# Kernel optimization log

Measured on AMD Instinct MI355X. Metric: run time of the kernel, lower is better.

## Reference

```python
import jax, jax.numpy as jnp
import numpy as np

N_HEADS, D_MODEL, D_HEAD = 16, 1024, 64
INIT_STD = 0.02


def setup_inputs() -> dict:
    key = jax.random.key(0)
    ks = jax.random.split(key, 5)
    x = jax.random.normal(ks[0], (4, 2048, D_MODEL), dtype=jnp.float32)
    W_Q = jax.random.normal(ks[1], (N_HEADS, D_MODEL, D_HEAD), dtype=jnp.float32) * INIT_STD
    W_K = jax.random.normal(ks[2], (N_HEADS, D_MODEL, D_HEAD), dtype=jnp.float32) * INIT_STD
    W_V = jax.random.normal(ks[3], (N_HEADS, D_MODEL, D_HEAD), dtype=jnp.float32) * INIT_STD
    W_O = jax.random.normal(ks[4], (N_HEADS, D_HEAD, D_MODEL), dtype=jnp.float32) * INIT_STD
    b_Q = jnp.zeros((N_HEADS, D_HEAD), dtype=jnp.float32)
    b_K = jnp.zeros((N_HEADS, D_HEAD), dtype=jnp.float32)
    b_V = jnp.zeros((N_HEADS, D_HEAD), dtype=jnp.float32)
    b_O = jnp.zeros((D_MODEL,), dtype=jnp.float32)
    return {"normalized_resid_pre": x, "W_Q": W_Q, "W_K": W_K, "W_V": W_V,
            "W_O": W_O, "b_Q": b_Q, "b_K": b_K, "b_V": b_V, "b_O": b_O}


def reference(normalized_resid_pre, W_Q, W_K, W_V, W_O, b_Q, b_K, b_V, b_O):
    x = normalized_resid_pre  # [b, s, d_model]
    q = jnp.einsum('bsm,hmd->bshd', x, W_Q) + b_Q  # [b, s, h, d_head]
    k = jnp.einsum('bsm,hmd->bshd', x, W_K) + b_K
    v = jnp.einsum('bsm,hmd->bshd', x, W_V) + b_V
    scores = jnp.einsum('bqhd,bkhd->bhqk', q, k) / jnp.sqrt(jnp.float32(D_HEAD))
    S = x.shape[1]
    causal = jnp.tril(jnp.ones((S, S), dtype=bool))  # keep key_pos <= query_pos
    scores = jnp.where(causal, scores, jnp.finfo(scores.dtype).min)
    pattern = jax.nn.softmax(scores, axis=-1)  # [b, h, q, k]
    z = jnp.einsum('bhqk,bkhd->bqhd', pattern, v)
    attn_out = jnp.einsum('bqhd,hdm->bqm', z, W_O) + b_O
    return attn_out
```

## Files before the change

### kernel.cpp

```cpp
#include <hip/hip_runtime.h>
#include <hip/hip_bf16.h>
#include <math.h>

typedef __bf16 bf16_t;
typedef bf16_t bf16x8 __attribute__((ext_vector_type(8)));
typedef float f32x4 __attribute__((ext_vector_type(4)));

#define BB 4
#define SS 2048
#define HH 16
#define DMODEL 1024
#define DHEAD 64

__device__ inline unsigned short f2bf(float f) {
    union { __hip_bfloat16 h; unsigned short u; } cvt;
    cvt.h = __float2bfloat16(f);
    return cvt.u;
}

__device__ __forceinline__ void gll16(const unsigned short* g, unsigned short* l) {
    __builtin_amdgcn_global_load_lds(
        (const __attribute__((address_space(1))) unsigned int*)(g),
        (__attribute__((address_space(3))) unsigned int*)(l), 16, 0, 0);
}


__global__ void pack_x(const float* __restrict__ x, unsigned short* __restrict__ xb) {
    int i = blockIdx.x * 256 + threadIdx.x;
    const float4 v = ((const float4*)x)[i];
    unsigned short o[4] = { f2bf(v.x), f2bf(v.y), f2bf(v.z), f2bf(v.w) };
    *(uint2*)(xb + 4 * (size_t)i) = *(uint2*)o;
}

__global__ void pack_wqkv(const float* __restrict__ wq, const float* __restrict__ wk,
                          const float* __restrict__ wv, unsigned short* __restrict__ out) {
    int idx = blockIdx.x * 256 + threadIdx.x;
    int k  = idx & 1023;
    int n  = idx >> 10;
    int mat = n >> 10;
    int n1 = n & 1023;
    int h = n1 >> 6, d = n1 & 63;
    const float* w = (mat == 0) ? wq : (mat == 1) ? wk : wv;
    out[idx] = f2bf(w[(h << 16) + (k << 6) + d]);
}

__global__ void pack_wo(const float* __restrict__ wo, unsigned short* __restrict__ out) {
    int idx = blockIdx.x * 256 + threadIdx.x;
    int k = idx & 1023, n = idx >> 10;
    out[idx] = f2bf(wo[(k << 10) + n]);
}


__global__ __launch_bounds__(256) void gemm_qkv(
    const unsigned short* __restrict__ xb,
    const unsigned short* __restrict__ wT,
    const float* __restrict__ bq, const float* __restrict__ bk, const float* __restrict__ bv,
    unsigned short* __restrict__ qws, unsigned short* __restrict__ kws,
    unsigned short* __restrict__ vtw)
{
    __shared__ __align__(16) unsigned short lA[128 * 32];
    __shared__ __align__(16) unsigned short lB[128 * 32];
    const int t = threadIdx.x;
    const int lane = t & 63;
    const int w = t >> 6;
    const int quad = lane >> 4;
    const int l15 = lane & 15;
    const int n0 = blockIdx.x * 128;
    const int m0 = blockIdx.y * 128;
    const int wm = (w >> 1) * 64;
    const int wn = (w & 1) * 64;
    const int mat = n0 >> 10;

    f32x4 acc[4][4] = {};

    const int srow = w * 16 + (lane >> 2);
    const int scol = (lane & 3) * 8;
    const unsigned short* Ag0 = xb + (size_t)(m0 + srow) * 1024 + scol;
    const unsigned short* Ag1 = Ag0 + (size_t)64 * 1024;
    const unsigned short* Bg0 = wT + (size_t)(n0 + srow) * 1024 + scol;
    const unsigned short* Bg1 = Bg0 + (size_t)64 * 1024;
    unsigned short* lA0 = lA + (w * 16) * 32;
    unsigned short* lA1 = lA + (64 + w * 16) * 32;
    unsigned short* lB0 = lB + (w * 16) * 32;
    unsigned short* lB1 = lB + (64 + w * 16) * 32;

    if (mat != 2) {
        for (int kt = 0; kt < 1024; kt += 32) {
            __syncthreads();
            gll16(Ag0 + kt, lA0);
            gll16(Ag1 + kt, lA1);
            gll16(Bg0 + kt, lB0);
            gll16(Bg1 + kt, lB1);
            __syncthreads();
            bf16x8 af[4], bfr[4];
#pragma unroll
            for (int i = 0; i < 4; i++) {
                af[i]  = *(const bf16x8*)(lA + (wm + i * 16 + l15) * 32 + quad * 8);
                bfr[i] = *(const bf16x8*)(lB + (wn + i * 16 + l15) * 32 + quad * 8);
            }
#pragma unroll
            for (int i = 0; i < 4; i++)
#pragma unroll
                for (int j = 0; j < 4; j++)
                    acc[i][j] = __builtin_amdgcn_mfma_f32_16x16x32_bf16(bfr[j], af[i], acc[i][j], 0, 0, 0);
        }
        const int b = m0 >> 11;
        const float* bias_p = (mat == 0) ? bq : bk;
        unsigned short* dst = (mat == 0) ? qws : kws;
#pragma unroll
        for (int j = 0; j < 4; j++) {
            const int noff = wn + j * 16 + quad * 4;
            const int h = noff >> 6;
            const int hglob = ((n0 & 1023) >> 6) + h;
            const int dbase = noff & 63;
            const float4 bv4 = *(const float4*)(bias_p + hglob * 64 + dbase);
            const float bias_r[4] = { bv4.x, bv4.y, bv4.z, bv4.w };
#pragma unroll
            for (int i = 0; i < 4; i++) {
                const int s = (m0 & 2047) + wm + i * 16 + l15;
                unsigned short pk[4];
#pragma unroll
                for (int r = 0; r < 4; r++) pk[r] = f2bf(acc[i][j][r] + bias_r[r]);
                *(uint2*)(dst + (size_t)((b * 16 + hglob) * 2048 + s) * 64 + dbase) = *(uint2*)pk;
            }
        }
    } else {
        for (int kt = 0; kt < 1024; kt += 32) {
            __syncthreads();
            gll16(Ag0 + kt, lA0);
            gll16(Ag1 + kt, lA1);
            gll16(Bg0 + kt, lB0);
            gll16(Bg1 + kt, lB1);
            __syncthreads();
            bf16x8 af[4], bfr[4];
#pragma unroll
            for (int i = 0; i < 4; i++) {
                af[i]  = *(const bf16x8*)(lA + (wm + i * 16 + l15) * 32 + quad * 8);
                bfr[i] = *(const bf16x8*)(lB + (wn + i * 16 + l15) * 32 + quad * 8);
            }
#pragma unroll
            for (int i = 0; i < 4; i++)
#pragma unroll
                for (int j = 0; j < 4; j++)
                    acc[i][j] = __builtin_amdgcn_mfma_f32_16x16x32_bf16(af[i], bfr[j], acc[i][j], 0, 0, 0);
        }
        const int b = m0 >> 11;
#pragma unroll
        for (int j = 0; j < 4; j++) {
            const int n1 = (n0 & 1023) + wn + j * 16 + l15;
            const int h = n1 >> 6, d = n1 & 63;
            const float bias = bv[h * 64 + d];
#pragma unroll
            for (int i = 0; i < 4; i++) {
                const int s0 = (m0 & 2047) + wm + i * 16 + quad * 4;
                unsigned short pk[4];
#pragma unroll
                for (int r = 0; r < 4; r++) pk[r] = f2bf(acc[i][j][r] + bias);
                *(uint2*)(vtw + ((size_t)(b * 16 + h) * 64 + d) * 2048 + s0) = *(uint2*)pk;
            }
        }
    }
}


__global__ __launch_bounds__(256) void attn3(
    const unsigned short* __restrict__ qws,
    const unsigned short* __restrict__ kws,
    const unsigned short* __restrict__ vtw,
    unsigned short* __restrict__ zb)
{
    __shared__ __align__(16) unsigned short Ks[64 * 72];
    __shared__ __align__(16) unsigned short Vs[64 * 72];
    __shared__ __align__(16) unsigned short Ps[4 * 16 * 72];

    const int t = threadIdx.x;
    const int lane = t & 63;
    const int w = t >> 6;
    const int quad = lane >> 4;
    const int l15 = lane & 15;

    const int qt = 31 - (blockIdx.x >> 6);
    const int bh = blockIdx.x & 63;
    const int q0 = qt * 64;
    const int qbase = q0 + w * 16;
    const size_t base = (size_t)bh * SS * DHEAD;
    const unsigned short* Q = qws + base;
    const unsigned short* K = kws + base;
    const unsigned short* Vt = vtw + base;

    bf16x8 qf0 = *(const bf16x8*)(Q + (size_t)(qbase + l15) * 64 + quad * 8);
    bf16x8 qf1 = *(const bf16x8*)(Q + (size_t)(qbase + l15) * 64 + 32 + quad * 8);

    f32x4 o[4] = {};
    float lsum[4] = {0.f, 0.f, 0.f, 0.f};
    unsigned short* Pw = Ps + w * 16 * 72;

    const int sr = t >> 2;
    const int sc = (t & 3) * 8;
    const int nch = qt + 1;

    for (int c = 0; c < nch; c++) {
        const int kb = c * 64;
        __syncthreads();
        {
            const unsigned short* kp = K + (size_t)(kb + sr) * 64 + sc;
            *(uint4*)(Ks + sr * 72 + sc)      = *(const uint4*)(kp);
            *(uint4*)(Ks + sr * 72 + sc + 32) = *(const uint4*)(kp + 32);
            const unsigned short* vp = Vt + (size_t)sr * 2048 + kb + sc;
            *(uint4*)(Vs + sr * 72 + sc)      = *(const uint4*)(vp);
            *(uint4*)(Vs + sr * 72 + sc + 32) = *(const uint4*)(vp + 32);
        }
        __syncthreads();

        f32x4 s[4];
#pragma unroll
        for (int sub = 0; sub < 4; sub++) {
            bf16x8 kf0 = *(const bf16x8*)(Ks + (sub * 16 + l15) * 72 + quad * 8);
            bf16x8 kf1 = *(const bf16x8*)(Ks + (sub * 16 + l15) * 72 + 32 + quad * 8);
            f32x4 sv = {};
            sv = __builtin_amdgcn_mfma_f32_16x16x32_bf16(qf0, kf0, sv, 0, 0, 0);
            sv = __builtin_amdgcn_mfma_f32_16x16x32_bf16(qf1, kf1, sv, 0, 0, 0);
            s[sub] = sv;
        }

        if (c == nch - 1) {
            const int qg = qbase + quad * 4;
#pragma unroll
            for (int sub = 0; sub < 4; sub++) {
                const int key = kb + sub * 16 + l15;
#pragma unroll
                for (int r = 0; r < 4; r++) {
                    float p = (key > qg + r) ? 0.f : __expf(s[sub][r] * 0.125f);
                    lsum[r] += p;
                    Pw[(quad * 4 + r) * 72 + sub * 16 + l15] = f2bf(p);
                }
            }
        } else {
#pragma unroll
            for (int sub = 0; sub < 4; sub++)
#pragma unroll
                for (int r = 0; r < 4; r++) {
                    float p = __expf(s[sub][r] * 0.125f);
                    lsum[r] += p;
                    Pw[(quad * 4 + r) * 72 + sub * 16 + l15] = f2bf(p);
                }
        }
        asm volatile("s_waitcnt lgkmcnt(0)" ::: "memory");
        bf16x8 pf0 = *(const bf16x8*)(Pw + l15 * 72 + quad * 8);
        bf16x8 pf1 = *(const bf16x8*)(Pw + l15 * 72 + 32 + quad * 8);
#pragma unroll
        for (int dt = 0; dt < 4; dt++) {
            bf16x8 vf0 = *(const bf16x8*)(Vs + (dt * 16 + l15) * 72 + quad * 8);
            bf16x8 vf1 = *(const bf16x8*)(Vs + (dt * 16 + l15) * 72 + 32 + quad * 8);
            o[dt] = __builtin_amdgcn_mfma_f32_16x16x32_bf16(vf0, pf0, o[dt], 0, 0, 0);
            o[dt] = __builtin_amdgcn_mfma_f32_16x16x32_bf16(vf1, pf1, o[dt], 0, 0, 0);
        }
    }

#pragma unroll
    for (int r = 0; r < 4; r++) {
        float v = lsum[r];
        v += __shfl_xor(v, 1);
        v += __shfl_xor(v, 2);
        v += __shfl_xor(v, 4);
        v += __shfl_xor(v, 8);
        lsum[r] = v;
    }
    const int srcl = (l15 >> 2) << 4;
    float t0 = __shfl(lsum[0], srcl);
    float t1 = __shfl(lsum[1], srcl);
    float t2 = __shfl(lsum[2], srcl);
    float t3 = __shfl(lsum[3], srcl);
    const int rr = l15 & 3;
    float den = (rr == 0) ? t0 : (rr == 1) ? t1 : (rr == 2) ? t2 : t3;
    const float inv = 1.0f / den;

    const int b = bh >> 4, h = bh & 15;
    const int q = qbase + l15;
    unsigned short* zrow = zb + (size_t)(b * 2048 + q) * 1024 + h * 64 + quad * 4;
#pragma unroll
    for (int dt = 0; dt < 4; dt++) {
        unsigned short pk[4];
#pragma unroll
        for (int r = 0; r < 4; r++) pk[r] = f2bf(o[dt][r] * inv);
        *(uint2*)(zrow + dt * 16) = *(uint2*)pk;
    }
}


__global__ __launch_bounds__(256) void gemm_out(
    const unsigned short* __restrict__ zb,
    const unsigned short* __restrict__ wT,
    const float* __restrict__ bo,
    float* __restrict__ out)
{
    __shared__ __align__(16) unsigned short lA[128 * 32];
    __shared__ __align__(16) unsigned short lB[128 * 32];
    const int t = threadIdx.x;
    const int lane = t & 63;
    const int w = t >> 6;
    const int quad = lane >> 4;
    const int l15 = lane & 15;
    const int n0 = blockIdx.x * 128;
    const int m0 = blockIdx.y * 128;
    const int wm = (w >> 1) * 64;
    const int wn = (w & 1) * 64;

    f32x4 acc[4][4] = {};

    const int srow = w * 16 + (lane >> 2);
    const int scol = (lane & 3) * 8;
    const unsigned short* Ag0 = zb + (size_t)(m0 + srow) * 1024 + scol;
    const unsigned short* Ag1 = Ag0 + (size_t)64 * 1024;
    const unsigned short* Bg0 = wT + (size_t)(n0 + srow) * 1024 + scol;
    const unsigned short* Bg1 = Bg0 + (size_t)64 * 1024;
    unsigned short* lA0 = lA + (w * 16) * 32;
    unsigned short* lA1 = lA + (64 + w * 16) * 32;
    unsigned short* lB0 = lB + (w * 16) * 32;
    unsigned short* lB1 = lB + (64 + w * 16) * 32;

    for (int kt = 0; kt < 1024; kt += 32) {
        __syncthreads();
        gll16(Ag0 + kt, lA0);
        gll16(Ag1 + kt, lA1);
        gll16(Bg0 + kt, lB0);
        gll16(Bg1 + kt, lB1);
        __syncthreads();
        bf16x8 af[4], bfr[4];
#pragma unroll
        for (int i = 0; i < 4; i++) {
            af[i]  = *(const bf16x8*)(lA + (wm + i * 16 + l15) * 32 + quad * 8);
            bfr[i] = *(const bf16x8*)(lB + (wn + i * 16 + l15) * 32 + quad * 8);
        }
#pragma unroll
        for (int i = 0; i < 4; i++)
#pragma unroll
            for (int j = 0; j < 4; j++)
                acc[i][j] = __builtin_amdgcn_mfma_f32_16x16x32_bf16(bfr[j], af[i], acc[i][j], 0, 0, 0);
    }

#pragma unroll
    for (int j = 0; j < 4; j++) {
        const int nbase = n0 + wn + j * 16 + quad * 4;
        const float4 bv4 = *(const float4*)(bo + nbase);
#pragma unroll
        for (int i = 0; i < 4; i++) {
            const int s = m0 + wm + i * 16 + l15;
            float4 v;
            v.x = acc[i][j][0] + bv4.x;
            v.y = acc[i][j][1] + bv4.y;
            v.z = acc[i][j][2] + bv4.z;
            v.w = acc[i][j][3] + bv4.w;
            *(float4*)(out + (size_t)s * 1024 + nbase) = v;
        }
    }
}


extern "C" void kernel_launch(void* const* d_in, const int* in_sizes, int n_in,
                              void* d_out, int out_size, void* d_ws, size_t ws_size,
                              hipStream_t stream) {
    const float* x  = (const float*)d_in[0];
    const float* WQ = (const float*)d_in[1];
    const float* WK = (const float*)d_in[2];
    const float* WV = (const float*)d_in[3];
    const float* WO = (const float*)d_in[4];
    const float* bQ = (const float*)d_in[5];
    const float* bK = (const float*)d_in[6];
    const float* bV = (const float*)d_in[7];
    const float* bO = (const float*)d_in[8];
    float* out = (float*)d_out;

    char* ws = (char*)d_ws;
    unsigned short* xb   = (unsigned short*)ws;
    unsigned short* wqkv = (unsigned short*)(ws + (16u << 20));
    unsigned short* woT  = (unsigned short*)(ws + (22u << 20));
    unsigned short* qws  = (unsigned short*)(ws + (24u << 20));
    unsigned short* kws  = (unsigned short*)(ws + (40u << 20));
    unsigned short* vtw  = (unsigned short*)(ws + (56u << 20));
    unsigned short* zbuf = xb;

    pack_x<<<8192, 256, 0, stream>>>(x, xb);
    pack_wqkv<<<(3072 * 1024) / 256, 256, 0, stream>>>(WQ, WK, WV, wqkv);
    pack_wo<<<(1024 * 1024) / 256, 256, 0, stream>>>(WO, woT);
    gemm_qkv<<<dim3(24, 64), 256, 0, stream>>>(xb, wqkv, bQ, bK, bV, qws, kws, vtw);
    attn3<<<2048, 256, 0, stream>>>(qws, kws, vtw, zbuf);
    gemm_out<<<dim3(8, 64), 256, 0, stream>>>(zbuf, woT, bO, out);
}
```

Baseline: 290.5 us.

## Fuse x conversion into QKV GEMM, merge weight packing, fold softmax scale

Drops the separate pack_x kernel. The QKV GEMM now loads fp32 x directly and converts it to bf16 while writing shared memory. The three weight pack kernels become one LDS-tiled transpose kernel with coalesced loads and stores. The softmax scale and log2(e) are folded into Q at its epilogue so attention can use exp2f. Both GEMMs also get a grouped block-index swizzle for L2 reuse, and the output GEMM's M tile shrinks to 64 to launch more blocks. The trade-off is that the x loads now go through registers instead of direct global-to-LDS loads, and x is reconverted by each of the 24 N-blocks.

```diff
diff --git a/kernel.cpp b/kernel.cpp
--- a/kernel.cpp
+++ b/kernel.cpp
@@ -11,6 +11,7 @@
 #define HH 16
 #define DMODEL 1024
 #define DHEAD 64
+#define QSCALE 0.18033688011112042f
 
 __device__ inline unsigned short f2bf(float f) {
     union { __hip_bfloat16 h; unsigned short u; } cvt;
@@ -24,35 +25,61 @@
         (__attribute__((address_space(3))) unsigned int*)(l), 16, 0, 0);
 }
 
-
-__global__ void pack_x(const float* __restrict__ x, unsigned short* __restrict__ xb) {
-    int i = blockIdx.x * 256 + threadIdx.x;
-    const float4 v = ((const float4*)x)[i];
-    unsigned short o[4] = { f2bf(v.x), f2bf(v.y), f2bf(v.z), f2bf(v.w) };
-    *(uint2*)(xb + 4 * (size_t)i) = *(uint2*)o;
-}
-
-__global__ void pack_wqkv(const float* __restrict__ wq, const float* __restrict__ wk,
-                          const float* __restrict__ wv, unsigned short* __restrict__ out) {
-    int idx = blockIdx.x * 256 + threadIdx.x;
-    int k  = idx & 1023;
-    int n  = idx >> 10;
-    int mat = n >> 10;
-    int n1 = n & 1023;
-    int h = n1 >> 6, d = n1 & 63;
-    const float* w = (mat == 0) ? wq : (mat == 1) ? wk : wv;
-    out[idx] = f2bf(w[(h << 16) + (k << 6) + d]);
-}
-
-__global__ void pack_wo(const float* __restrict__ wo, unsigned short* __restrict__ out) {
-    int idx = blockIdx.x * 256 + threadIdx.x;
-    int k = idx & 1023, n = idx >> 10;
-    out[idx] = f2bf(wo[(k << 10) + n]);
+__global__ __launch_bounds__(256) void pack_w(
+    const float* __restrict__ wq, const float* __restrict__ wk, const float* __restrict__ wv,
+    const float* __restrict__ wo, unsigned short* __restrict__ qkvT, unsigned short* __restrict__ woT)
+{
+    __shared__ unsigned short tile[64 * 72];
+    const int t = threadIdx.x;
+    const int bid = blockIdx.x;
+    const int r = t >> 2;
+    const int c4 = (t & 3) * 16;
+    if (bid < 768) {
+        const int mat = bid >> 8;
+        const int rem = bid & 255;
+        const int h = rem >> 4;
+        const int m0 = (rem & 15) * 64;
+        const float* w = (mat == 0) ? wq : (mat == 1) ? wk : wv;
+        const float* src = w + ((size_t)h << 16) + (size_t)(m0 + r) * 64 + c4;
+#pragma unroll
+        for (int k2 = 0; k2 < 4; k2++) {
+            float4 v = *(const float4*)(src + k2 * 4);
+            tile[(c4 + k2 * 4 + 0) * 72 + r] = f2bf(v.x);
+            tile[(c4 + k2 * 4 + 1) * 72 + r] = f2bf(v.y);
+            tile[(c4 + k2 * 4 + 2) * 72 + r] = f2bf(v.z);
+            tile[(c4 + k2 * 4 + 3) * 72 + r] = f2bf(v.w);
+        }
+        __syncthreads();
+        const int d = t >> 2;
+        const int rq = (t & 3) * 16;
+        unsigned short* dst = qkvT + (size_t)(mat * 1024 + h * 64 + d) * 1024 + m0 + rq;
+        *(uint4*)(dst)     = *(const uint4*)(tile + d * 72 + rq);
+        *(uint4*)(dst + 8) = *(const uint4*)(tile + d * 72 + rq + 8);
+    } else {
+        const int bid2 = bid - 768;
+        const int h = bid2 >> 4;
+        const int m0 = (bid2 & 15) * 64;
+        const float* src = wo + ((size_t)h << 16) + (size_t)r * 1024 + m0 + c4;
+#pragma unroll
+        for (int k2 = 0; k2 < 4; k2++) {
+            float4 v = *(const float4*)(src + k2 * 4);
+            tile[(c4 + k2 * 4 + 0) * 72 + r] = f2bf(v.x);
+            tile[(c4 + k2 * 4 + 1) * 72 + r] = f2bf(v.y);
+            tile[(c4 + k2 * 4 + 2) * 72 + r] = f2bf(v.z);
+            tile[(c4 + k2 * 4 + 3) * 72 + r] = f2bf(v.w);
+        }
+        __syncthreads();
+        const int m = t >> 2;
+        const int dq = (t & 3) * 16;
+        unsigned short* dst = woT + (size_t)(m0 + m) * 1024 + h * 64 + dq;
+        *(uint4*)(dst)     = *(const uint4*)(tile + m * 72 + dq);
+        *(uint4*)(dst + 8) = *(const uint4*)(tile + m * 72 + dq + 8);
+    }
 }
 
 
 __global__ __launch_bounds__(256) void gemm_qkv(
-    const unsigned short* __restrict__ xb,
+    const float* __restrict__ xg,
     const unsigned short* __restrict__ wT,
     const float* __restrict__ bq, const float* __restrict__ bk, const float* __restrict__ bv,
     unsigned short* __restrict__ qws, unsigned short* __restrict__ kws,
@@ -65,8 +92,11 @@
     const int w = t >> 6;
     const int quad = lane >> 4;
     const int l15 = lane & 15;
-    const int n0 = blockIdx.x * 128;
-    const int m0 = blockIdx.y * 128;
+    const int bid = blockIdx.x;
+    const int mb = (bid & 7) + ((bid / 192) << 3);
+    const int nb = (bid >> 3) % 24;
+    const int n0 = nb * 128;
+    const int m0 = mb * 128;
     const int wm = (w >> 1) * 64;
     const int wn = (w & 1) * 64;
     const int mat = n0 >> 10;
@@ -75,43 +105,62 @@
 
     const int srow = w * 16 + (lane >> 2);
     const int scol = (lane & 3) * 8;
-    const unsigned short* Ag0 = xb + (size_t)(m0 + srow) * 1024 + scol;
-    const unsigned short* Ag1 = Ag0 + (size_t)64 * 1024;
+    const float* Ax0 = xg + (size_t)(m0 + srow) * 1024 + scol;
+    const float* Ax1 = Ax0 + (size_t)64 * 1024;
     const unsigned short* Bg0 = wT + (size_t)(n0 + srow) * 1024 + scol;
     const unsigned short* Bg1 = Bg0 + (size_t)64 * 1024;
-    unsigned short* lA0 = lA + (w * 16) * 32;
-    unsigned short* lA1 = lA + (64 + w * 16) * 32;
+    unsigned short* lAd0 = lA + srow * 32 + scol;
+    unsigned short* lAd1 = lA + (64 + srow) * 32 + scol;
     unsigned short* lB0 = lB + (w * 16) * 32;
     unsigned short* lB1 = lB + (64 + w * 16) * 32;
 
-    if (mat != 2) {
-        for (int kt = 0; kt < 1024; kt += 32) {
-            __syncthreads();
-            gll16(Ag0 + kt, lA0);
-            gll16(Ag1 + kt, lA1);
-            gll16(Bg0 + kt, lB0);
-            gll16(Bg1 + kt, lB1);
-            __syncthreads();
-            bf16x8 af[4], bfr[4];
-#pragma unroll
-            for (int i = 0; i < 4; i++) {
-                af[i]  = *(const bf16x8*)(lA + (wm + i * 16 + l15) * 32 + quad * 8);
-                bfr[i] = *(const bf16x8*)(lB + (wn + i * 16 + l15) * 32 + quad * 8);
-            }
+    for (int kt = 0; kt < 1024; kt += 32) {
+        __syncthreads();
+        {
+            float4 u0 = *(const float4*)(Ax0 + kt);
+            float4 u1 = *(const float4*)(Ax0 + kt + 4);
+            float4 u2 = *(const float4*)(Ax1 + kt);
+            float4 u3 = *(const float4*)(Ax1 + kt + 4);
+            unsigned short p0[8] = { f2bf(u0.x), f2bf(u0.y), f2bf(u0.z), f2bf(u0.w),
+                                     f2bf(u1.x), f2bf(u1.y), f2bf(u1.z), f2bf(u1.w) };
+            unsigned short p1[8] = { f2bf(u2.x), f2bf(u2.y), f2bf(u2.z), f2bf(u2.w),
+                                     f2bf(u3.x), f2bf(u3.y), f2bf(u3.z), f2bf(u3.w) };
+            *(uint4*)lAd0 = *(uint4*)p0;
+            *(uint4*)lAd1 = *(uint4*)p1;
+        }
+        gll16(Bg0 + kt, lB0);
+        gll16(Bg1 + kt, lB1);
+        __syncthreads();
+        bf16x8 af[4], bfr[4];
+#pragma unroll
+        for (int i = 0; i < 4; i++) {
+            af[i]  = *(const bf16x8*)(lA + (wm + i * 16 + l15) * 32 + quad * 8);
+            bfr[i] = *(const bf16x8*)(lB + (wn + i * 16 + l15) * 32 + quad * 8);
+        }
+        if (mat != 2) {
 #pragma unroll
             for (int i = 0; i < 4; i++)
 #pragma unroll
                 for (int j = 0; j < 4; j++)
                     acc[i][j] = __builtin_amdgcn_mfma_f32_16x16x32_bf16(bfr[j], af[i], acc[i][j], 0, 0, 0);
-        }
-        const int b = m0 >> 11;
+        } else {
+#pragma unroll
+            for (int i = 0; i < 4; i++)
+#pragma unroll
+                for (int j = 0; j < 4; j++)
+                    acc[i][j] = __builtin_amdgcn_mfma_f32_16x16x32_bf16(af[i], bfr[j], acc[i][j], 0, 0, 0);
+        }
+    }
+
+    const int b = m0 >> 11;
+    if (mat != 2) {
         const float* bias_p = (mat == 0) ? bq : bk;
         unsigned short* dst = (mat == 0) ? qws : kws;
+        const float qscale = (mat == 0) ? QSCALE : 1.0f;
 #pragma unroll
         for (int j = 0; j < 4; j++) {
             const int noff = wn + j * 16 + quad * 4;
-            const int h = noff >> 6;
-            const int hglob = ((n0 & 1023) >> 6) + h;
+            const int hglob = ((n0 & 1023) >> 6) + (noff >> 6);
             const int dbase = noff & 63;
             const float4 bv4 = *(const float4*)(bias_p + hglob * 64 + dbase);
             const float bias_r[4] = { bv4.x, bv4.y, bv4.z, bv4.w };
@@ -120,31 +169,11 @@
                 const int s = (m0 & 2047) + wm + i * 16 + l15;
                 unsigned short pk[4];
 #pragma unroll
-                for (int r = 0; r < 4; r++) pk[r] = f2bf(acc[i][j][r] + bias_r[r]);
+                for (int r = 0; r < 4; r++) pk[r] = f2bf((acc[i][j][r] + bias_r[r]) * qscale);
                 *(uint2*)(dst + (size_t)((b * 16 + hglob) * 2048 + s) * 64 + dbase) = *(uint2*)pk;
             }
         }
     } else {
-        for (int kt = 0; kt < 1024; kt += 32) {
-            __syncthreads();
-            gll16(Ag0 + kt, lA0);
-            gll16(Ag1 + kt, lA1);
-            gll16(Bg0 + kt, lB0);
-            gll16(Bg1 + kt, lB1);
-            __syncthreads();
-            bf16x8 af[4], bfr[4];
-#pragma unroll
-            for (int i = 0; i < 4; i++) {
-                af[i]  = *(const bf16x8*)(lA + (wm + i * 16 + l15) * 32 + quad * 8);
-                bfr[i] = *(const bf16x8*)(lB + (wn + i * 16 + l15) * 32 + quad * 8);
-            }
-#pragma unroll
-            for (int i = 0; i < 4; i++)
-#pragma unroll
-                for (int j = 0; j < 4; j++)
-                    acc[i][j] = __builtin_amdgcn_mfma_f32_16x16x32_bf16(af[i], bfr[j], acc[i][j], 0, 0, 0);
-        }
-        const int b = m0 >> 11;
 #pragma unroll
         for (int j = 0; j < 4; j++) {
             const int n1 = (n0 & 1023) + wn + j * 16 + l15;
@@ -230,7 +259,7 @@
                 const int key = kb + sub * 16 + l15;
 #pragma unroll
                 for (int r = 0; r < 4; r++) {
-                    float p = (key > qg + r) ? 0.f : __expf(s[sub][r] * 0.125f);
+                    float p = (key > qg + r) ? 0.f : exp2f(s[sub][r]);
                     lsum[r] += p;
                     Pw[(quad * 4 + r) * 72 + sub * 16 + l15] = f2bf(p);
                 }
@@ -240,7 +269,7 @@
             for (int sub = 0; sub < 4; sub++)
 #pragma unroll
                 for (int r = 0; r < 4; r++) {
-                    float p = __expf(s[sub][r] * 0.125f);
+                    float p = exp2f(s[sub][r]);
                     lsum[r] += p;
                     Pw[(quad * 4 + r) * 72 + sub * 16 + l15] = f2bf(p);
                 }
@@ -294,46 +323,47 @@
     const float* __restrict__ bo,
     float* __restrict__ out)
 {
-    __shared__ __align__(16) unsigned short lA[128 * 32];
+    __shared__ __align__(16) unsigned short lA[64 * 32];
     __shared__ __align__(16) unsigned short lB[128 * 32];
     const int t = threadIdx.x;
     const int lane = t & 63;
     const int w = t >> 6;
     const int quad = lane >> 4;
     const int l15 = lane & 15;
-    const int n0 = blockIdx.x * 128;
-    const int m0 = blockIdx.y * 128;
-    const int wm = (w >> 1) * 64;
+    const int bid = blockIdx.x;
+    const int mb = (bid & 7) + ((bid >> 6) << 3);
+    const int nb = (bid >> 3) & 7;
+    const int n0 = nb * 128;
+    const int m0 = mb * 64;
+    const int wm = (w >> 1) * 32;
     const int wn = (w & 1) * 64;
 
-    f32x4 acc[4][4] = {};
+    f32x4 acc[2][4] = {};
 
     const int srow = w * 16 + (lane >> 2);
     const int scol = (lane & 3) * 8;
     const unsigned short* Ag0 = zb + (size_t)(m0 + srow) * 1024 + scol;
-    const unsigned short* Ag1 = Ag0 + (size_t)64 * 1024;
     const unsigned short* Bg0 = wT + (size_t)(n0 + srow) * 1024 + scol;
     const unsigned short* Bg1 = Bg0 + (size_t)64 * 1024;
     unsigned short* lA0 = lA + (w * 16) * 32;
-    unsigned short* lA1 = lA + (64 + w * 16) * 32;
     unsigned short* lB0 = lB + (w * 16) * 32;
     unsigned short* lB1 = lB + (64 + w * 16) * 32;
 
     for (int kt = 0; kt < 1024; kt += 32) {
         __syncthreads();
         gll16(Ag0 + kt, lA0);
-        gll16(Ag1 + kt, lA1);
         gll16(Bg0 + kt, lB0);
         gll16(Bg1 + kt, lB1);
         __syncthreads();
-        bf16x8 af[4], bfr[4];
-#pragma unroll
-        for (int i = 0; i < 4; i++) {
+        bf16x8 af[2], bfr[4];
+#pragma unroll
+        for (int i = 0; i < 2; i++)
             af[i]  = *(const bf16x8*)(lA + (wm + i * 16 + l15) * 32 + quad * 8);
-            bfr[i] = *(const bf16x8*)(lB + (wn + i * 16 + l15) * 32 + quad * 8);
-        }
-#pragma unroll
-        for (int i = 0; i < 4; i++)
+#pragma unroll
+        for (int j = 0; j < 4; j++)
+            bfr[j] = *(const bf16x8*)(lB + (wn + j * 16 + l15) * 32 + quad * 8);
+#pragma unroll
+        for (int i = 0; i < 2; i++)
 #pragma unroll
             for (int j = 0; j < 4; j++)
                 acc[i][j] = __builtin_amdgcn_mfma_f32_16x16x32_bf16(bfr[j], af[i], acc[i][j], 0, 0, 0);
@@ -344,7 +374,7 @@
         const int nbase = n0 + wn + j * 16 + quad * 4;
         const float4 bv4 = *(const float4*)(bo + nbase);
 #pragma unroll
-        for (int i = 0; i < 4; i++) {
+        for (int i = 0; i < 2; i++) {
             const int s = m0 + wm + i * 16 + l15;
             float4 v;
             v.x = acc[i][j][0] + bv4.x;
@@ -372,18 +402,15 @@
     float* out = (float*)d_out;
 
     char* ws = (char*)d_ws;
-    unsigned short* xb   = (unsigned short*)ws;
+    unsigned short* zbuf = (unsigned short*)ws;
     unsigned short* wqkv = (unsigned short*)(ws + (16u << 20));
     unsigned short* woT  = (unsigned short*)(ws + (22u << 20));
     unsigned short* qws  = (unsigned short*)(ws + (24u << 20));
     unsigned short* kws  = (unsigned short*)(ws + (40u << 20));
     unsigned short* vtw  = (unsigned short*)(ws + (56u << 20));
-    unsigned short* zbuf = xb;
-
-    pack_x<<<8192, 256, 0, stream>>>(x, xb);
-    pack_wqkv<<<(3072 * 1024) / 256, 256, 0, stream>>>(WQ, WK, WV, wqkv);
-    pack_wo<<<(1024 * 1024) / 256, 256, 0, stream>>>(WO, woT);
-    gemm_qkv<<<dim3(24, 64), 256, 0, stream>>>(xb, wqkv, bQ, bK, bV, qws, kws, vtw);
+
+    pack_w<<<1024, 256, 0, stream>>>(WQ, WK, WV, WO, wqkv, woT);
+    gemm_qkv<<<1536, 256, 0, stream>>>(x, wqkv, bQ, bK, bV, qws, kws, vtw);
     attn3<<<2048, 256, 0, stream>>>(qws, kws, vtw, zbuf);
-    gemm_out<<<dim3(8, 64), 256, 0, stream>>>(zbuf, woT, bO, out);
-}
+    gemm_out<<<1024, 256, 0, stream>>>(zbuf, woT, bO, out);
+}
```

Result: slower. 332.7 us (+14.5%).
